# Performance work log

Hardware: AMD Instinct MI355X
Metric: run time of the kernel (lower is better)

Reference implementation:

```python
import jax, jax.numpy as jnp
import numpy as np

NX = 1024
N_HEAD = 16
HEAD_DIM = NX // N_HEAD
MASKED_BIAS = -10000.0


def setup_inputs() -> dict:
    key = jax.random.key(0)
    k1, k2, k3 = jax.random.split(key, 3)
    hidden_states = jax.random.normal(k1, (2, 2048, NX), dtype=jnp.float32)
    # Conv1D weights: stored [in, out], y = x @ W + b (like torch addmm)
    c_attn_w = jax.random.normal(k2, (NX, 3 * NX), dtype=jnp.float32) * 0.02
    c_attn_b = jnp.zeros((3 * NX,), dtype=jnp.float32)
    c_proj_w = jax.random.normal(k3, (NX, NX), dtype=jnp.float32) * 0.02
    c_proj_b = jnp.zeros((NX,), dtype=jnp.float32)
    return {
        "hidden_states": hidden_states,
        "c_attn_w": c_attn_w,
        "c_attn_b": c_attn_b,
        "c_proj_w": c_proj_w,
        "c_proj_b": c_proj_b,
    }


def reference(hidden_states, c_attn_w, c_attn_b, c_proj_w, c_proj_b):
    B, S, _ = hidden_states.shape
    qkv = hidden_states @ c_attn_w + c_attn_b  # [B, S, 3*NX]
    q, k, v = jnp.split(qkv, 3, axis=-1)
    # split heads -> [B, H, S, D]
    def split_heads(x):
        return x.reshape(B, S, N_HEAD, HEAD_DIM).transpose(0, 2, 1, 3)
    q, k, v = split_heads(q), split_heads(k), split_heads(v)
    # scores scaled by sqrt(head_dim) (v.size(-1)**0.5 in original)
    w = jnp.einsum("bhqd,bhkd->bhqk", q, k) / jnp.sqrt(jnp.float32(HEAD_DIM))
    # causal mask (nd == ns here since no past)
    causal = jnp.tril(jnp.ones((S, S), dtype=bool))
    w = jnp.where(causal[None, None, :, :], w, jnp.float32(MASKED_BIAS))
    w = jax.nn.softmax(w, axis=-1)
    a = jnp.einsum("bhqk,bhkd->bhqd", w, v)  # [B, H, S, D]
    # merge heads
    a = a.transpose(0, 2, 1, 3).reshape(B, S, NX)
    out = a @ c_proj_w + c_proj_b
    return out
```

## Files before the change

### kernel.cpp

```cpp
#include <hip/hip_runtime.h>
#include <hip/hip_bf16.h>
#include <cmath>

typedef __attribute__((ext_vector_type(8))) short bf16x8;
typedef __attribute__((ext_vector_type(4))) float f32x4;

#define NXC 1024
#define NH 16
#define HD 64
#define BATCH 2
#define SEQ 2048
#define TOK (BATCH * SEQ)

__device__ __forceinline__ ushort f2bf(float f) {
  unsigned u;
  asm("v_cvt_pk_bf16_f32 %0, %1, %2" : "=v"(u) : "v"(f), "v"(f));
  return (ushort)u;
}

__device__ __forceinline__ void gload_lds16(const void* g, void* lds) {
  __builtin_amdgcn_global_load_lds(
      (const __attribute__((address_space(1))) void*)g,
      (__attribute__((address_space(3))) void*)lds, 16, 0, 0);
}

__device__ __forceinline__ float fast_exp2(float x) {
  float r;
  asm("v_exp_f32 %0, %1" : "=v"(r) : "v"(x));
  return r;
}

template <int CTRL>
__device__ __forceinline__ float dpp_mov(float x) {
  return __builtin_bit_cast(
      float, __builtin_amdgcn_mov_dpp(__builtin_bit_cast(int, x), CTRL, 0xF, 0xF, true));
}
__device__ __forceinline__ float red16_max(float x) {
  x = fmaxf(x, dpp_mov<0x121>(x));
  x = fmaxf(x, dpp_mov<0x122>(x));
  x = fmaxf(x, dpp_mov<0x124>(x));
  x = fmaxf(x, dpp_mov<0x128>(x));
  return x;
}
__device__ __forceinline__ float red16_sum(float x) {
  x += dpp_mov<0x121>(x);
  x += dpp_mov<0x122>(x);
  x += dpp_mov<0x124>(x);
  x += dpp_mov<0x128>(x);
  return x;
}

__global__ __launch_bounds__(256) void k_transpose_w(const float* __restrict__ in,
                                                     ushort* __restrict__ out,
                                                     int Kd, int Nd) {
  __shared__ float t[32][33];
  int n0 = blockIdx.x * 32, k0 = blockIdx.y * 32;
  int tx = threadIdx.x & 31, ty = threadIdx.x >> 5;
#pragma unroll
  for (int r = 0; r < 4; ++r)
    t[tx][ty + r * 8] = in[(size_t)(k0 + ty + r * 8) * Nd + n0 + tx];
  __syncthreads();
  int nl = threadIdx.x >> 3, kq = (threadIdx.x & 7) * 4;
  ushort4 o;
  o.x = f2bf(t[nl][kq + 0]);
  o.y = f2bf(t[nl][kq + 1]);
  o.z = f2bf(t[nl][kq + 2]);
  o.w = f2bf(t[nl][kq + 3]);
  int row = n0 + nl, kk = k0 + kq;
  size_t dst = (size_t)row * Kd + (kk & ~63) + ((kk & 63) ^ ((row & 7) << 3));
  *(ushort4*)&out[dst] = o;
}

__global__ __launch_bounds__(256) void k_transpose_v(const ushort* __restrict__ in,
                                                     ushort* __restrict__ out) {
  __shared__ ushort t[64][33];
  int bh = blockIdx.z;
  int s0 = blockIdx.x * 64, d0 = blockIdx.y * 32;
  const ushort* ip = in + (size_t)bh * SEQ * HD;
  ushort* op = out + (size_t)bh * HD * SEQ;
  int dl_in = threadIdx.x & 31, sl_in = threadIdx.x >> 5;
#pragma unroll
  for (int m = 0; m < 8; ++m)
    t[sl_in + m * 8][dl_in] = ip[(size_t)(s0 + sl_in + m * 8) * HD + d0 + dl_in];
  __syncthreads();
  int dl = threadIdx.x >> 3;
  int kp = threadIdx.x & 7;
#pragma unroll
  for (int kk = 0; kk < 2; ++kk) {
    int k = kp * 2 + kk;
    ushort4 o;
    o.x = t[k][dl]; o.y = t[k + 16][dl]; o.z = t[k + 32][dl]; o.w = t[k + 48][dl];
    int slot = (4 * k) ^ ((dl & 7) << 3);
    *(ushort4*)&op[(size_t)(d0 + dl) * SEQ + s0 + slot] = o;
  }
}

__global__ __launch_bounds__(256, 3) void k_gemm_qkv(const float* __restrict__ X,
                                                     const ushort* __restrict__ Bt,
                                                     const float* __restrict__ bias,
                                                     ushort* __restrict__ q_ws,
                                                     ushort* __restrict__ k_ws,
                                                     ushort* __restrict__ v_tmp) {
  __shared__ ushort As[128 * 64];
  __shared__ ushort Bs[2][128 * 64];
  const int tid = threadIdx.x;
  const int wave = tid >> 6, lane = tid & 63;
  const int xcd = blockIdx.x & 7, loc = blockIdx.x >> 3;
  const int m0 = ((xcd >> 1) * 8 + (loc & 7)) * 128;
  const int n0 = ((xcd & 1) * 12 + (loc >> 3)) * 128;
  const int wr = (wave >> 1) * 64, wc = (wave & 1) * 64;
  const int l15 = lane & 15, lg = lane >> 4;
  const int swz = (l15 & 7) << 3;
  const int arow = wave * 32 + lg;
  const int akcol = l15 * 4;
  f32x4 acc[4][4] = {};
  float4 areg[8];

  auto a_issue = [&](int kt) {
#pragma unroll
    for (int c = 0; c < 8; ++c)
      areg[c] = *(const float4*)&X[(size_t)(m0 + arow + c * 4) * 1024 + kt * 64 + akcol];
  };
  auto a_write = [&]() {
#pragma unroll
    for (int c = 0; c < 8; ++c) {
      int row = arow + c * 4;
      unsigned p0, p1;
      asm("v_cvt_pk_bf16_f32 %0, %1, %2" : "=v"(p0) : "v"(areg[c].x), "v"(areg[c].y));
      asm("v_cvt_pk_bf16_f32 %0, %1, %2" : "=v"(p1) : "v"(areg[c].z), "v"(areg[c].w));
      *(uint2*)&As[row * 64 + (akcol ^ ((row & 7) << 3))] = make_uint2(p0, p1);
    }
  };
  auto stageB = [&](int kt, int buf) {
#pragma unroll
    for (int c = 0; c < 4; ++c) {
      int offB = wave * 4096 + c * 1024 + lane * 16;
      int row = offB >> 7, colB = offB & 127;
      gload_lds16((const char*)Bt + (size_t)(n0 + row) * 2048 + kt * 128 + colB,
                  (char*)Bs[buf] + wave * 4096 + c * 1024);
    }
  };

  a_issue(0);
  stageB(0, 0);
  a_write();
  a_issue(1);
  asm volatile("s_waitcnt vmcnt(8) lgkmcnt(0)" ::: "memory");
  __builtin_amdgcn_s_barrier();

#pragma unroll 1
  for (int kt = 0; kt < 16; ++kt) {
    const int cur = kt & 1;
    if (kt < 15) stageB(kt + 1, cur ^ 1);
#pragma unroll
    for (int kc = 0; kc < 2; ++kc) {
      bf16x8 af[4], bfr[4];
#pragma unroll
      for (int i = 0; i < 4; ++i)
        af[i] = *(const bf16x8*)&As[(wr + i * 16 + l15) * 64 + ((kc * 32 + lg * 8) ^ swz)];
#pragma unroll
      for (int j = 0; j < 4; ++j)
        bfr[j] = *(const bf16x8*)&Bs[cur][(wc + j * 16 + l15) * 64 + ((kc * 32 + lg * 8) ^ swz)];
#pragma unroll
      for (int i = 0; i < 4; ++i)
#pragma unroll
        for (int j = 0; j < 4; ++j)
          acc[i][j] = __builtin_amdgcn_mfma_f32_16x16x32_bf16(af[i], bfr[j], acc[i][j], 0, 0, 0);
    }
    __syncthreads();
    if (kt < 15) {
      a_write();
      if (kt < 14) a_issue(kt + 2);
      asm volatile("s_waitcnt lgkmcnt(0)" ::: "memory");
      __builtin_amdgcn_s_barrier();
    }
  }

#pragma unroll
  for (int j = 0; j < 4; ++j) {
    int col = n0 + wc + j * 16 + l15;
    float bv = bias[col];
    int sec = col >> 10;
    int within = col & 1023;
    int head = within >> 6, d = within & 63;
#pragma unroll
    for (int i = 0; i < 4; ++i) {
#pragma unroll
      for (int r = 0; r < 4; ++r) {
        int row = m0 + wr + i * 16 + lg * 4 + r;
        int b = row >> 11, s = row & 2047;
        float val = acc[i][j][r] + bv;
        size_t hb = ((size_t)(b * NH + head) * SEQ + s) * HD;
        if (sec == 0)      q_ws[hb + d] = f2bf(val * 0.1803368801f);
        else if (sec == 1) k_ws[hb + (d ^ ((s & 7) << 3))] = f2bf(val);
        else               v_tmp[hb + d] = f2bf(val);
      }
    }
  }
}

__global__ __launch_bounds__(256) void k_attn(const ushort* __restrict__ q_ws,
                                              const ushort* __restrict__ k_ws,
                                              const ushort* __restrict__ v_ws,
                                              ushort* __restrict__ a_ws) {
  __shared__ ushort Ks[2][64 * 64];
  __shared__ ushort Vs[2][64 * 64];
  __shared__ ushort Ps[4][2][16 * 64];
  const int bid = blockIdx.x;
  const int xcd = bid & 7, idx = bid >> 3;
  const int bh = xcd * 4 + (idx >> 4);
  const int p = idx & 15;
  const int qtA = 31 - p, qtB = p;
  const int tid = threadIdx.x, wave = tid >> 6, lane = tid & 63;
  const int l15 = lane & 15, lg = lane >> 4;
  const int swz = (l15 & 7) << 3;
  const ushort* qp = q_ws + (size_t)bh * SEQ * HD;
  const ushort* kp = k_ws + (size_t)bh * SEQ * HD;
  const ushort* vp = v_ws + (size_t)bh * HD * SEQ;

  bf16x8 qfA[2], qfB[2];
  {
    int qrA = qtA * 64 + wave * 16 + l15;
    int qrB = qtB * 64 + wave * 16 + l15;
    qfA[0] = *(const bf16x8*)&qp[(size_t)qrA * HD + lg * 8];
    qfA[1] = *(const bf16x8*)&qp[(size_t)qrA * HD + 32 + lg * 8];
    qfB[0] = *(const bf16x8*)&qp[(size_t)qrB * HD + lg * 8];
    qfB[1] = *(const bf16x8*)&qp[(size_t)qrB * HD + 32 + lg * 8];
  }
  f32x4 oA[4] = {}, oB[4] = {};
  float mA[4] = {-INFINITY, -INFINITY, -INFINITY, -INFINITY};
  float mB[4] = {-INFINITY, -INFINITY, -INFINITY, -INFINITY};
  float lA[4] = {0.f, 0.f, 0.f, 0.f}, lB[4] = {0.f, 0.f, 0.f, 0.f};
  bf16x8 kf[2][4], vf[2][4];

  auto stage = [&](int kt, int buf) {
#pragma unroll
    for (int c = 0; c < 2; ++c) {
      int offB = wave * 2048 + c * 1024 + lane * 16;
      gload_lds16((const char*)kp + (size_t)kt * 8192 + offB,
                  (char*)Ks[buf] + offB);
      int d = offB >> 7, keyB = offB & 127;
      gload_lds16((const char*)vp + (size_t)d * (SEQ * 2) + (size_t)kt * 128 + keyB,
                  (char*)Vs[buf] + offB);
    }
  };

  auto tile_step = [&](const bf16x8* qf, f32x4* o, float* m_r, float* l_r,
                       ushort* Pw, bool diag) {
    f32x4 sc[4] = {};
    __builtin_amdgcn_s_setprio(1);
#pragma unroll
    for (int kc = 0; kc < 2; ++kc)
#pragma unroll
      for (int f = 0; f < 4; ++f) {
        if (diag && f > wave) continue;
        sc[f] = __builtin_amdgcn_mfma_f32_16x16x32_bf16(qf[kc], kf[kc][f], sc[f], 0, 0, 0);
      }
    __builtin_amdgcn_s_setprio(0);
    if (diag) {
#pragma unroll
      for (int f = 0; f < 4; ++f) {
        int key_rel = f * 16 + l15;
#pragma unroll
        for (int r = 0; r < 4; ++r) {
          int q_rel = wave * 16 + lg * 4 + r;
          if (key_rel > q_rel) sc[f][r] = -1e30f;
        }
      }
    }
    float pm[4];
#pragma unroll
    for (int r = 0; r < 4; ++r)
      pm[r] = fmaxf(fmaxf(sc[0][r], sc[1][r]), fmaxf(sc[2][r], sc[3][r]));
    bool need = false;
#pragma unroll
    for (int r = 0; r < 4; ++r) need |= (pm[r] > m_r[r] + 8.f);
    if (__any(need)) {
#pragma unroll
      for (int r = 0; r < 4; ++r) {
        float full = red16_max(pm[r]);
        float mn = fmaxf(m_r[r], full);
        float al = fast_exp2(m_r[r] - mn);
        m_r[r] = mn;
        l_r[r] *= al;
#pragma unroll
        for (int df = 0; df < 4; ++df) o[df][r] *= al;
      }
    }
#pragma unroll
    for (int r = 0; r < 4; ++r) {
      int q = lg * 4 + r;
      float e0 = fast_exp2(sc[0][r] - m_r[r]);
      float e1 = fast_exp2(sc[1][r] - m_r[r]);
      float e2 = fast_exp2(sc[2][r] - m_r[r]);
      float e3 = fast_exp2(sc[3][r] - m_r[r]);
      l_r[r] += (e0 + e1) + (e2 + e3);
      unsigned p0, p1;
      asm("v_cvt_pk_bf16_f32 %0, %1, %2" : "=v"(p0) : "v"(e0), "v"(e1));
      asm("v_cvt_pk_bf16_f32 %0, %1, %2" : "=v"(p1) : "v"(e2), "v"(e3));
      *(uint2*)&Pw[q * 64 + ((l15 * 4) ^ ((q & 7) << 3))] = make_uint2(p0, p1);
    }
    __builtin_amdgcn_s_setprio(1);
#pragma unroll
    for (int kc = 0; kc < 2; ++kc) {
      bf16x8 pf = *(const bf16x8*)&Pw[l15 * 64 + ((kc * 32 + lg * 8) ^ swz)];
#pragma unroll
      for (int df = 0; df < 4; ++df)
        o[df] = __builtin_amdgcn_mfma_f32_16x16x32_bf16(pf, vf[kc][df], o[df], 0, 0, 0);
    }
    __builtin_amdgcn_s_setprio(0);
  };

  stage(0, 0);
  asm volatile("s_waitcnt vmcnt(0)" ::: "memory");
  __syncthreads();

  for (int kt = 0; kt <= qtA; ++kt) {
    const int cur = kt & 1;
    if (kt < qtA) stage(kt + 1, cur ^ 1);
#pragma unroll
    for (int kc = 0; kc < 2; ++kc)
#pragma unroll
      for (int f = 0; f < 4; ++f) {
        kf[kc][f] = *(const bf16x8*)&Ks[cur][(f * 16 + l15) * 64 + ((kc * 32 + lg * 8) ^ swz)];
        vf[kc][f] = *(const bf16x8*)&Vs[cur][(f * 16 + l15) * 64 + ((kc * 32 + lg * 8) ^ swz)];
      }
    tile_step(qfA, oA, mA, lA, Ps[wave][0], kt == qtA);
    if (kt <= qtB)
      tile_step(qfB, oB, mB, lB, Ps[wave][1], kt == qtB);
    asm volatile("s_waitcnt vmcnt(0)" ::: "memory");
    __builtin_amdgcn_s_barrier();
  }

  int b = bh >> 4, head = bh & 15;
  auto epilogue = [&](f32x4* o, float* l_r, int qt) {
#pragma unroll
    for (int r = 0; r < 4; ++r) {
      float inv = 1.0f / red16_sum(l_r[r]);
      int s = qt * 64 + wave * 16 + lg * 4 + r;
#pragma unroll
      for (int df = 0; df < 4; ++df) {
        int col = head * 64 + ((df * 16 + l15) ^ ((s & 7) << 3));
        a_ws[((size_t)(b * SEQ + s)) * NXC + col] = f2bf(o[df][r] * inv);
      }
    }
  };
  epilogue(oA, lA, qtA);
  epilogue(oB, lB, qtB);
}

__global__ __launch_bounds__(256) void k_gemm_proj(const ushort* __restrict__ A,
                                                   const ushort* __restrict__ Bt,
                                                   const float* __restrict__ bias,
                                                   float* __restrict__ out) {
  __shared__ ushort As[2][128 * 64];
  __shared__ ushort Bs[2][128 * 64];
  const int tid = threadIdx.x;
  const int wave = tid >> 6, lane = tid & 63;
  const int xcd = blockIdx.x & 7, loc = blockIdx.x >> 3;
  const int m0 = ((xcd >> 1) * 8 + (loc & 7)) * 128;
  const int n0 = ((xcd & 1) * 4 + (loc >> 3)) * 128;
  const int wr = (wave >> 1) * 64, wc = (wave & 1) * 64;
  const int l15 = lane & 15, lg = lane >> 4;
  const int swz = (l15 & 7) << 3;
  f32x4 acc[4][4] = {};

  auto stage = [&](int k0, int buf) {
#pragma unroll
    for (int c = 0; c < 4; ++c) {
      int offB = wave * 4096 + c * 1024 + lane * 16;
      int row = offB >> 7, colB = offB & 127;
      gload_lds16((const char*)A + (size_t)(m0 + row) * 2048 + k0 * 2 + colB,
                  (char*)As[buf] + wave * 4096 + c * 1024);
      gload_lds16((const char*)Bt + (size_t)(n0 + row) * 2048 + k0 * 2 + colB,
                  (char*)Bs[buf] + wave * 4096 + c * 1024);
    }
  };

  stage(0, 0);
  asm volatile("s_waitcnt vmcnt(0)" ::: "memory");
  __syncthreads();

  for (int kt = 0; kt < 16; ++kt) {
    const int cur = kt & 1;
    if (kt < 15) stage((kt + 1) * 64, cur ^ 1);
#pragma unroll
    for (int kc = 0; kc < 2; ++kc) {
      bf16x8 af[4], bfr[4];
#pragma unroll
      for (int i = 0; i < 4; ++i)
        af[i] = *(const bf16x8*)&As[cur][(wr + i * 16 + l15) * 64 + ((kc * 32 + lg * 8) ^ swz)];
#pragma unroll
      for (int j = 0; j < 4; ++j)
        bfr[j] = *(const bf16x8*)&Bs[cur][(wc + j * 16 + l15) * 64 + ((kc * 32 + lg * 8) ^ swz)];
#pragma unroll
      for (int i = 0; i < 4; ++i)
#pragma unroll
        for (int j = 0; j < 4; ++j)
          acc[i][j] = __builtin_amdgcn_mfma_f32_16x16x32_bf16(af[i], bfr[j], acc[i][j], 0, 0, 0);
    }
    asm volatile("s_waitcnt vmcnt(0)" ::: "memory");
    __syncthreads();
  }
#pragma unroll
  for (int j = 0; j < 4; ++j) {
    int col = n0 + wc + j * 16 + l15;
    float bv = bias[col];
#pragma unroll
    for (int i = 0; i < 4; ++i) {
#pragma unroll
      for (int r = 0; r < 4; ++r) {
        int row = m0 + wr + i * 16 + lg * 4 + r;
        out[(size_t)row * NXC + col] = acc[i][j][r] + bv;
      }
    }
  }
}

extern "C" void kernel_launch(void* const* d_in, const int* in_sizes, int n_in,
                              void* d_out, int out_size, void* d_ws, size_t ws_size,
                              hipStream_t stream) {
  const float* hs       = (const float*)d_in[0];
  const float* c_attn_w = (const float*)d_in[1];
  const float* c_attn_b = (const float*)d_in[2];
  const float* c_proj_w = (const float*)d_in[3];
  const float* c_proj_b = (const float*)d_in[4];
  char* ws = (char*)d_ws;
  const size_t MB = 1 << 20;
  ushort* Wt_attn = (ushort*)(ws + 8 * MB);
  ushort* Wt_proj = (ushort*)(ws + 14 * MB);
  ushort* q_ws    = (ushort*)(ws + 16 * MB);
  ushort* k_ws    = (ushort*)(ws + 24 * MB);
  ushort* v_ws    = (ushort*)(ws + 32 * MB);
  ushort* a_ws    = (ushort*)(ws + 40 * MB);
  ushort* v_tmp   = a_ws;

  k_transpose_w<<<dim3(96, 32), 256, 0, stream>>>(c_attn_w, Wt_attn, 1024, 3072);
  k_transpose_w<<<dim3(32, 32), 256, 0, stream>>>(c_proj_w, Wt_proj, 1024, 1024);
  k_gemm_qkv<<<768, 256, 0, stream>>>(hs, Wt_attn, c_attn_b, q_ws, k_ws, v_tmp);
  k_transpose_v<<<dim3(32, 2, 32), 256, 0, stream>>>(v_tmp, v_ws);
  k_attn<<<512, 256, 0, stream>>>(q_ws, k_ws, v_ws, a_ws);
  k_gemm_proj<<<256, 256, 0, stream>>>(a_ws, Wt_proj, c_proj_b, (float*)d_out);
}
```

Measured before the change: 123.3 us.

## Split paired query tiles across two wave groups in 512-thread attention blocks

Measured after the change: 145.0 us. 1.18x slower.

```diff
diff --git a/kernel.cpp b/kernel.cpp
--- a/kernel.cpp
+++ b/kernel.cpp
@@ -199,116 +199,44 @@
   }
 }
 
-__global__ __launch_bounds__(256) void k_attn(const ushort* __restrict__ q_ws,
+__global__ __launch_bounds__(512) void k_attn(const ushort* __restrict__ q_ws,
                                               const ushort* __restrict__ k_ws,
                                               const ushort* __restrict__ v_ws,
                                               ushort* __restrict__ a_ws) {
   __shared__ ushort Ks[2][64 * 64];
   __shared__ ushort Vs[2][64 * 64];
-  __shared__ ushort Ps[4][2][16 * 64];
+  __shared__ ushort Ps[8][16 * 64];
   const int bid = blockIdx.x;
   const int xcd = bid & 7, idx = bid >> 3;
   const int bh = xcd * 4 + (idx >> 4);
   const int p = idx & 15;
   const int qtA = 31 - p, qtB = p;
   const int tid = threadIdx.x, wave = tid >> 6, lane = tid & 63;
+  const int grp = wave >> 2, w4 = wave & 3;
   const int l15 = lane & 15, lg = lane >> 4;
   const int swz = (l15 & 7) << 3;
+  const int qt = grp == 0 ? qtA : qtB;
   const ushort* qp = q_ws + (size_t)bh * SEQ * HD;
   const ushort* kp = k_ws + (size_t)bh * SEQ * HD;
   const ushort* vp = v_ws + (size_t)bh * HD * SEQ;
-
-  bf16x8 qfA[2], qfB[2];
+  ushort* Pw = Ps[wave];
+
+  bf16x8 qf[2];
   {
-    int qrA = qtA * 64 + wave * 16 + l15;
-    int qrB = qtB * 64 + wave * 16 + l15;
-    qfA[0] = *(const bf16x8*)&qp[(size_t)qrA * HD + lg * 8];
-    qfA[1] = *(const bf16x8*)&qp[(size_t)qrA * HD + 32 + lg * 8];
-    qfB[0] = *(const bf16x8*)&qp[(size_t)qrB * HD + lg * 8];
-    qfB[1] = *(const bf16x8*)&qp[(size_t)qrB * HD + 32 + lg * 8];
-  }
-  f32x4 oA[4] = {}, oB[4] = {};
-  float mA[4] = {-INFINITY, -INFINITY, -INFINITY, -INFINITY};
-  float mB[4] = {-INFINITY, -INFINITY, -INFINITY, -INFINITY};
-  float lA[4] = {0.f, 0.f, 0.f, 0.f}, lB[4] = {0.f, 0.f, 0.f, 0.f};
-  bf16x8 kf[2][4], vf[2][4];
+    int qrow = qt * 64 + w4 * 16 + l15;
+    qf[0] = *(const bf16x8*)&qp[(size_t)qrow * HD + lg * 8];
+    qf[1] = *(const bf16x8*)&qp[(size_t)qrow * HD + 32 + lg * 8];
+  }
+  f32x4 o[4] = {};
+  float m_r[4] = {-INFINITY, -INFINITY, -INFINITY, -INFINITY};
+  float l_r[4] = {0.f, 0.f, 0.f, 0.f};
 
   auto stage = [&](int kt, int buf) {
-#pragma unroll
-    for (int c = 0; c < 2; ++c) {
-      int offB = wave * 2048 + c * 1024 + lane * 16;
-      gload_lds16((const char*)kp + (size_t)kt * 8192 + offB,
-                  (char*)Ks[buf] + offB);
-      int d = offB >> 7, keyB = offB & 127;
-      gload_lds16((const char*)vp + (size_t)d * (SEQ * 2) + (size_t)kt * 128 + keyB,
-                  (char*)Vs[buf] + offB);
-    }
-  };
-
-  auto tile_step = [&](const bf16x8* qf, f32x4* o, float* m_r, float* l_r,
-                       ushort* Pw, bool diag) {
-    f32x4 sc[4] = {};
-    __builtin_amdgcn_s_setprio(1);
-#pragma unroll
-    for (int kc = 0; kc < 2; ++kc)
-#pragma unroll
-      for (int f = 0; f < 4; ++f) {
-        if (diag && f > wave) continue;
-        sc[f] = __builtin_amdgcn_mfma_f32_16x16x32_bf16(qf[kc], kf[kc][f], sc[f], 0, 0, 0);
-      }
-    __builtin_amdgcn_s_setprio(0);
-    if (diag) {
-#pragma unroll
-      for (int f = 0; f < 4; ++f) {
-        int key_rel = f * 16 + l15;
-#pragma unroll
-        for (int r = 0; r < 4; ++r) {
-          int q_rel = wave * 16 + lg * 4 + r;
-          if (key_rel > q_rel) sc[f][r] = -1e30f;
-        }
-      }
-    }
-    float pm[4];
-#pragma unroll
-    for (int r = 0; r < 4; ++r)
-      pm[r] = fmaxf(fmaxf(sc[0][r], sc[1][r]), fmaxf(sc[2][r], sc[3][r]));
-    bool need = false;
-#pragma unroll
-    for (int r = 0; r < 4; ++r) need |= (pm[r] > m_r[r] + 8.f);
-    if (__any(need)) {
-#pragma unroll
-      for (int r = 0; r < 4; ++r) {
-        float full = red16_max(pm[r]);
-        float mn = fmaxf(m_r[r], full);
-        float al = fast_exp2(m_r[r] - mn);
-        m_r[r] = mn;
-        l_r[r] *= al;
-#pragma unroll
-        for (int df = 0; df < 4; ++df) o[df][r] *= al;
-      }
-    }
-#pragma unroll
-    for (int r = 0; r < 4; ++r) {
-      int q = lg * 4 + r;
-      float e0 = fast_exp2(sc[0][r] - m_r[r]);
-      float e1 = fast_exp2(sc[1][r] - m_r[r]);
-      float e2 = fast_exp2(sc[2][r] - m_r[r]);
-      float e3 = fast_exp2(sc[3][r] - m_r[r]);
-      l_r[r] += (e0 + e1) + (e2 + e3);
-      unsigned p0, p1;
-      asm("v_cvt_pk_bf16_f32 %0, %1, %2" : "=v"(p0) : "v"(e0), "v"(e1));
-      asm("v_cvt_pk_bf16_f32 %0, %1, %2" : "=v"(p1) : "v"(e2), "v"(e3));
-      *(uint2*)&Pw[q * 64 + ((l15 * 4) ^ ((q & 7) << 3))] = make_uint2(p0, p1);
-    }
-    __builtin_amdgcn_s_setprio(1);
-#pragma unroll
-    for (int kc = 0; kc < 2; ++kc) {
-      bf16x8 pf = *(const bf16x8*)&Pw[l15 * 64 + ((kc * 32 + lg * 8) ^ swz)];
-#pragma unroll
-      for (int df = 0; df < 4; ++df)
-        o[df] = __builtin_amdgcn_mfma_f32_16x16x32_bf16(pf, vf[kc][df], o[df], 0, 0, 0);
-    }
-    __builtin_amdgcn_s_setprio(0);
+    int off = tid * 16;
+    gload_lds16((const char*)kp + (size_t)kt * 8192 + off, (char*)Ks[buf] + off);
+    int d = off >> 7, colB = off & 127;
+    gload_lds16((const char*)vp + (size_t)d * (SEQ * 2) + (size_t)kt * 128 + colB,
+                (char*)Vs[buf] + off);
   };
 
   stage(0, 0);
@@ -318,35 +246,94 @@
   for (int kt = 0; kt <= qtA; ++kt) {
     const int cur = kt & 1;
     if (kt < qtA) stage(kt + 1, cur ^ 1);
-#pragma unroll
-    for (int kc = 0; kc < 2; ++kc)
-#pragma unroll
-      for (int f = 0; f < 4; ++f) {
-        kf[kc][f] = *(const bf16x8*)&Ks[cur][(f * 16 + l15) * 64 + ((kc * 32 + lg * 8) ^ swz)];
-        vf[kc][f] = *(const bf16x8*)&Vs[cur][(f * 16 + l15) * 64 + ((kc * 32 + lg * 8) ^ swz)];
-      }
-    tile_step(qfA, oA, mA, lA, Ps[wave][0], kt == qtA);
-    if (kt <= qtB)
-      tile_step(qfB, oB, mB, lB, Ps[wave][1], kt == qtB);
+    if (kt <= qt) {
+      const bool diag = (kt == qt);
+      bf16x8 kf[2][4], vf[2][4];
+#pragma unroll
+      for (int kc = 0; kc < 2; ++kc)
+#pragma unroll
+        for (int f = 0; f < 4; ++f) {
+          kf[kc][f] = *(const bf16x8*)&Ks[cur][(f * 16 + l15) * 64 + ((kc * 32 + lg * 8) ^ swz)];
+          vf[kc][f] = *(const bf16x8*)&Vs[cur][(f * 16 + l15) * 64 + ((kc * 32 + lg * 8) ^ swz)];
+        }
+      f32x4 sc[4] = {};
+      __builtin_amdgcn_s_setprio(1);
+#pragma unroll
+      for (int kc = 0; kc < 2; ++kc)
+#pragma unroll
+        for (int f = 0; f < 4; ++f) {
+          if (diag && f > w4) continue;
+          sc[f] = __builtin_amdgcn_mfma_f32_16x16x32_bf16(qf[kc], kf[kc][f], sc[f], 0, 0, 0);
+        }
+      __builtin_amdgcn_s_setprio(0);
+      if (diag) {
+#pragma unroll
+        for (int f = 0; f < 4; ++f) {
+          int key_rel = f * 16 + l15;
+#pragma unroll
+          for (int r = 0; r < 4; ++r) {
+            int q_rel = w4 * 16 + lg * 4 + r;
+            if (key_rel > q_rel) sc[f][r] = -1e30f;
+          }
+        }
+      }
+      float pm[4];
+#pragma unroll
+      for (int r = 0; r < 4; ++r)
+        pm[r] = fmaxf(fmaxf(sc[0][r], sc[1][r]), fmaxf(sc[2][r], sc[3][r]));
+      bool need = false;
+#pragma unroll
+      for (int r = 0; r < 4; ++r) need |= (pm[r] > m_r[r] + 8.f);
+      if (__any(need)) {
+#pragma unroll
+        for (int r = 0; r < 4; ++r) {
+          float full = red16_max(pm[r]);
+          float mn = fmaxf(m_r[r], full);
+          float al = fast_exp2(m_r[r] - mn);
+          m_r[r] = mn;
+          l_r[r] *= al;
+#pragma unroll
+          for (int df = 0; df < 4; ++df) o[df][r] *= al;
+        }
+      }
+#pragma unroll
+      for (int r = 0; r < 4; ++r) {
+        int q = lg * 4 + r;
+        float e0 = fast_exp2(sc[0][r] - m_r[r]);
+        float e1 = fast_exp2(sc[1][r] - m_r[r]);
+        float e2 = fast_exp2(sc[2][r] - m_r[r]);
+        float e3 = fast_exp2(sc[3][r] - m_r[r]);
+        l_r[r] += (e0 + e1) + (e2 + e3);
+        unsigned p0, p1;
+        asm("v_cvt_pk_bf16_f32 %0, %1, %2" : "=v"(p0) : "v"(e0), "v"(e1));
+        asm("v_cvt_pk_bf16_f32 %0, %1, %2" : "=v"(p1) : "v"(e2), "v"(e3));
+        *(uint2*)&Pw[q * 64 + ((l15 * 4) ^ ((q & 7) << 3))] = make_uint2(p0, p1);
+      }
+      __builtin_amdgcn_s_setprio(1);
+#pragma unroll
+      for (int kc = 0; kc < 2; ++kc) {
+        bf16x8 pf = *(const bf16x8*)&Pw[l15 * 64 + ((kc * 32 + lg * 8) ^ swz)];
+#pragma unroll
+        for (int df = 0; df < 4; ++df)
+          o[df] = __builtin_amdgcn_mfma_f32_16x16x32_bf16(pf, vf[kc][df], o[df], 0, 0, 0);
+      }
+      __builtin_amdgcn_s_setprio(0);
+    }
     asm volatile("s_waitcnt vmcnt(0)" ::: "memory");
     __builtin_amdgcn_s_barrier();
   }
 
   int b = bh >> 4, head = bh & 15;
-  auto epilogue = [&](f32x4* o, float* l_r, int qt) {
-#pragma unroll
-    for (int r = 0; r < 4; ++r) {
-      float inv = 1.0f / red16_sum(l_r[r]);
-      int s = qt * 64 + wave * 16 + lg * 4 + r;
-#pragma unroll
-      for (int df = 0; df < 4; ++df) {
-        int col = head * 64 + ((df * 16 + l15) ^ ((s & 7) << 3));
-        a_ws[((size_t)(b * SEQ + s)) * NXC + col] = f2bf(o[df][r] * inv);
-      }
-    }
-  };
-  epilogue(oA, lA, qtA);
-  epilogue(oB, lB, qtB);
+#pragma unroll
+  for (int r = 0; r < 4; ++r) {
+    float inv = 1.0f / red16_sum(l_r[r]);
+    int s = qt * 64 + w4 * 16 + lg * 4 + r;
+#pragma unroll
+    for (int df = 0; df < 4; ++df) {
+      int col = head * 64 + ((df * 16 + l15) ^ ((s & 7) << 3));
+      a_ws[((size_t)(b * SEQ + s)) * NXC + col] = f2bf(o[df][r] * inv);
+    }
+  }
 }
 
 __global__ __launch_bounds__(256) void k_gemm_proj(const ushort* __restrict__ A,
@@ -439,6 +426,6 @@
   k_transpose_w<<<dim3(32, 32), 256, 0, stream>>>(c_proj_w, Wt_proj, 1024, 1024);
   k_gemm_qkv<<<768, 256, 0, stream>>>(hs, Wt_attn, c_attn_b, q_ws, k_ws, v_tmp);
   k_transpose_v<<<dim3(32, 2, 32), 256, 0, stream>>>(v_tmp, v_ws);
-  k_attn<<<512, 256, 0, stream>>>(q_ws, k_ws, v_ws, a_ws);
+  k_attn<<<512, 512, 0, stream>>>(q_ws, k_ws, v_ws, a_ws);
   k_gemm_proj<<<256, 256, 0, stream>>>(a_ws, Wt_proj, c_proj_b, (float*)d_out);
 }
```
